# Kernel optimization log

Hardware: AMD Instinct MI355X
Metric: run time of the kernel (lower is better)

Reference implementation:

```python
import jax, jax.numpy as jnp
import numpy as np

KH = KW = 3
STRIDE = 2
PAD = 1


def _extract_patches(x, kh, kw, stride, pad):
    # x: [B, C, H, W] -> patches [B, C, Ho, Wo, kh*kw]
    B, C, H, W = x.shape
    xp = jnp.pad(x, ((0, 0), (0, 0), (pad, pad), (pad, pad)))
    Ho = (H + 2 * pad - kh) // stride + 1
    Wo = (W + 2 * pad - kw) // stride + 1
    cols = [
        xp[:, :, i : i + stride * Ho : stride, j : j + stride * Wo : stride]
        for i in range(kh)
        for j in range(kw)
    ]
    return jnp.stack(cols, axis=-1)  # [B, C, Ho, Wo, kh*kw]


def setup_inputs() -> dict:
    key = jax.random.key(0)
    k1, k2 = jax.random.split(key)
    x = jax.random.normal(k1, (32, 64, 112, 112), dtype=jnp.float32)
    s = jax.random.normal(k2, (64, KH, KW), dtype=jnp.float32) * 0.1
    return {"x": x, "s": s}


def reference(x, s):
    # RRSVM rank-weighted pooling: for each sliding window, sort values
    # descending and take a weighted sum with per-channel rank weights s.
    patches = _extract_patches(x, KH, KW, STRIDE, PAD)  # [B,C,Ho,Wo,K]
    order = jnp.argsort(-patches, axis=-1)              # descending ranks
    sorted_vals = jnp.take_along_axis(patches, order, axis=-1)
    s_flat = s.reshape(s.shape[0], KH * KW)             # [C, K]
    out = jnp.einsum("bchwk,ck->bchw", sorted_vals, s_flat)
    return out, order.astype(jnp.int64)
```

## Files before the change

kernel.cpp:

```cpp
#include <hip/hip_runtime.h>


typedef float nfloat4 __attribute__((ext_vector_type(4)));

constexpr int B  = 32;
constexpr int C  = 64;
constexpr int H  = 112;
constexpr int W  = 112;
constexpr int HO = 56;
constexpr int WO = 56;
constexpr int KK = 9;
constexpr int NPIX = HO * WO;
constexpr int BLK  = 256;
constexpr int LROW = 128;
constexpr int RPT  = 4;
constexpr int IR   = 2 * RPT + 1;

__global__ __launch_bounds__(BLK) void rrsvm_kernel(
    const float* __restrict__ x, const float* __restrict__ s,
    float* __restrict__ out, float* __restrict__ order)
{
    __shared__ float lx[IR * LROW];
    __shared__ float lorder[RPT * WO * KK];

    const int plane = blockIdx.y;
    const int ho0   = blockIdx.x;
    const int tid   = threadIdx.x;
    const int w     = tid >> 6;
    const int lane  = tid & 63;
    const int c     = plane & (C - 1);

    const float* xp = x + (size_t)plane * (H * W);

    if (tid < IR * (W / 4)) {
        const int r  = tid / (W / 4);
        const int cc = tid - r * (W / 4);
        const int grow = 8 * ho0 - 1 + r;
        nfloat4 val = (nfloat4)0.0f;
        if ((unsigned)grow < (unsigned)H)
            val = *(const nfloat4*)(xp + grow * W + 4 * cc);
        float* dst = &lx[r * LROW + 1 + 4 * cc];
        dst[0] = val.x; dst[1] = val.y; dst[2] = val.z; dst[3] = val.w;
    }
    if (tid < IR) lx[tid * LROW] = 0.0f;
    __syncthreads();

    const bool live = (lane < WO);
    const int  lc   = live ? lane : 0;
    const int  ho   = ho0 * RPT + w;

    float v[KK];
    float fid[KK];
#pragma unroll
    for (int dy = 0; dy < 3; ++dy)
#pragma unroll
        for (int dx = 0; dx < 3; ++dx) {
            const int k = dy * 3 + dx;
            v[k]   = lx[(2 * w + dy) * LROW + 2 * lc + dx];
            fid[k] = (float)k;
        }

    auto CE = [&](int a, int b) {
        const float va = v[a],   vb = v[b];
        const float fa = fid[a], fb = fid[b];
        const bool sw = (va < vb) || ((va == vb) && (fa > fb));
        v[a]   = sw ? vb : va;  v[b]   = sw ? va : vb;
        fid[a] = sw ? fb : fa;  fid[b] = sw ? fa : fb;
    };
    CE(0,1); CE(2,3); CE(4,5); CE(6,7);
    CE(0,2); CE(1,3); CE(4,6); CE(5,7);
    CE(1,2); CE(5,6);
    CE(0,4); CE(1,5); CE(2,6); CE(3,7);
    CE(2,4); CE(3,5);
    CE(1,2); CE(3,4); CE(5,6);
    CE(7,8); CE(6,7); CE(5,6); CE(4,5); CE(3,4); CE(2,3); CE(1,2); CE(0,1);

    const float* sc = s + c * KK;
    float acc = 0.0f;
#pragma unroll
    for (int k = 0; k < KK; ++k) acc = fmaf(v[k], sc[k], acc);

    if (live) {
        __builtin_nontemporal_store(acc, out + (size_t)plane * NPIX + ho * WO + lane);
        const int widx = w * WO + lane;
#pragma unroll
        for (int k = 0; k < KK; ++k)
            lorder[widx * KK + k] = fid[k];
    }
    __syncthreads();

    nfloat4* __restrict__ ob =
        (nfloat4*)(order + ((size_t)plane * NPIX + (size_t)ho0 * RPT * WO) * KK);
    const nfloat4* __restrict__ lb = (const nfloat4*)lorder;
#pragma unroll
    for (int i = tid; i < RPT * WO * KK / 4; i += BLK)
        __builtin_nontemporal_store(lb[i], ob + i);
}

extern "C" void kernel_launch(void* const* d_in, const int* in_sizes, int n_in,
                              void* d_out, int out_size, void* d_ws, size_t ws_size,
                              hipStream_t stream) {
    const float* x = (const float*)d_in[0];
    const float* s = (const float*)d_in[1];
    float* out   = (float*)d_out;
    float* order = out + (size_t)B * C * NPIX;

    dim3 grid(HO / RPT, B * C);
    rrsvm_kernel<<<grid, dim3(BLK), 0, stream>>>(x, s, out, order);
}
```

Baseline: 313.3 us.

## Make each block loop over all row tiles of a plane with double-buffered staging

The grid changes from one block per (row-tile, plane) to one persistent block per plane, which iterates over all 14 row tiles. The next tile's input rows are prefetched into registers during compute and written to the alternate LDS buffer, so load latency can overlap with sorting and stores. Per-channel weights are loaded once per block, and the halo rows between tiles are re-read. The cost is a grid of only 2048 blocks, which means less parallelism and longer-running blocks, plus two barriers per iteration.

```diff
diff --git a/kernel.cpp b/kernel.cpp
--- a/kernel.cpp
+++ b/kernel.cpp
@@ -15,16 +15,16 @@
 constexpr int LROW = 128;
 constexpr int RPT  = 4;
 constexpr int IR   = 2 * RPT + 1;
+constexpr int NT   = HO / RPT;
 
-__global__ __launch_bounds__(BLK) void rrsvm_kernel(
+__global__ __launch_bounds__(BLK, 8) void rrsvm_kernel(
     const float* __restrict__ x, const float* __restrict__ s,
     float* __restrict__ out, float* __restrict__ order)
 {
-    __shared__ float lx[IR * LROW];
+    __shared__ float lx[2][IR * LROW];
     __shared__ float lorder[RPT * WO * KK];
 
-    const int plane = blockIdx.y;
-    const int ho0   = blockIdx.x;
+    const int plane = blockIdx.x;
     const int tid   = threadIdx.x;
     const int w     = tid >> 6;
     const int lane  = tid & 63;
@@ -32,69 +32,94 @@
 
     const float* xp = x + (size_t)plane * (H * W);
 
-    if (tid < IR * (W / 4)) {
-        const int r  = tid / (W / 4);
-        const int cc = tid - r * (W / 4);
-        const int grow = 8 * ho0 - 1 + r;
+    const bool stager = (tid < IR * (W / 4));
+    const int  sr  = tid / (W / 4);
+    const int  scc = tid - sr * (W / 4);
+
+    float wts[KK];
+#pragma unroll
+    for (int k = 0; k < KK; ++k) wts[k] = s[c * KK + k];
+
+    if (tid < 2 * IR) {
+        const int bi = tid / IR, r = tid - bi * IR;
+        lx[bi][r * LROW] = 0.0f;
+    }
+
+    if (stager) {
+        const int grow = sr - 1;
         nfloat4 val = (nfloat4)0.0f;
         if ((unsigned)grow < (unsigned)H)
-            val = *(const nfloat4*)(xp + grow * W + 4 * cc);
-        float* dst = &lx[r * LROW + 1 + 4 * cc];
+            val = *(const nfloat4*)(xp + grow * W + 4 * scc);
+        float* dst = &lx[0][sr * LROW + 1 + 4 * scc];
         dst[0] = val.x; dst[1] = val.y; dst[2] = val.z; dst[3] = val.w;
     }
-    if (tid < IR) lx[tid * LROW] = 0.0f;
     __syncthreads();
 
     const bool live = (lane < WO);
     const int  lc   = live ? lane : 0;
-    const int  ho   = ho0 * RPT + w;
 
-    float v[KK];
-    float fid[KK];
-#pragma unroll
-    for (int dy = 0; dy < 3; ++dy)
-#pragma unroll
-        for (int dx = 0; dx < 3; ++dx) {
-            const int k = dy * 3 + dx;
-            v[k]   = lx[(2 * w + dy) * LROW + 2 * lc + dx];
-            fid[k] = (float)k;
+    for (int t = 0; t < NT; ++t) {
+        nfloat4 nval = (nfloat4)0.0f;
+        if (t + 1 < NT && stager) {
+            const int grow = 8 * (t + 1) - 1 + sr;
+            nval = *(const nfloat4*)(xp + grow * W + 4 * scc);
         }
 
-    auto CE = [&](int a, int b) {
-        const float va = v[a],   vb = v[b];
-        const float fa = fid[a], fb = fid[b];
-        const bool sw = (va < vb) || ((va == vb) && (fa > fb));
-        v[a]   = sw ? vb : va;  v[b]   = sw ? va : vb;
-        fid[a] = sw ? fb : fa;  fid[b] = sw ? fa : fb;
-    };
-    CE(0,1); CE(2,3); CE(4,5); CE(6,7);
-    CE(0,2); CE(1,3); CE(4,6); CE(5,7);
-    CE(1,2); CE(5,6);
-    CE(0,4); CE(1,5); CE(2,6); CE(3,7);
-    CE(2,4); CE(3,5);
-    CE(1,2); CE(3,4); CE(5,6);
-    CE(7,8); CE(6,7); CE(5,6); CE(4,5); CE(3,4); CE(2,3); CE(1,2); CE(0,1);
+        const float* lxt = lx[t & 1];
+        float v[KK];
+        float fid[KK];
+#pragma unroll
+        for (int dy = 0; dy < 3; ++dy)
+#pragma unroll
+            for (int dx = 0; dx < 3; ++dx) {
+                const int k = dy * 3 + dx;
+                v[k]   = lxt[(2 * w + dy) * LROW + 2 * lc + dx];
+                fid[k] = (float)k;
+            }
 
-    const float* sc = s + c * KK;
-    float acc = 0.0f;
+        auto CE = [&](int a, int b) {
+            const float va = v[a],   vb = v[b];
+            const float fa = fid[a], fb = fid[b];
+            const bool sw = (va < vb) || ((va == vb) && (fa > fb));
+            v[a]   = sw ? vb : va;  v[b]   = sw ? va : vb;
+            fid[a] = sw ? fb : fa;  fid[b] = sw ? fa : fb;
+        };
+        CE(0,1); CE(2,3); CE(4,5); CE(6,7);
+        CE(0,2); CE(1,3); CE(4,6); CE(5,7);
+        CE(1,2); CE(5,6);
+        CE(0,4); CE(1,5); CE(2,6); CE(3,7);
+        CE(2,4); CE(3,5);
+        CE(1,2); CE(3,4); CE(5,6);
+        CE(7,8); CE(6,7); CE(5,6); CE(4,5); CE(3,4); CE(2,3); CE(1,2); CE(0,1);
+
+        float acc = 0.0f;
 #pragma unroll
-    for (int k = 0; k < KK; ++k) acc = fmaf(v[k], sc[k], acc);
+        for (int k = 0; k < KK; ++k) acc = fmaf(v[k], wts[k], acc);
 
-    if (live) {
-        __builtin_nontemporal_store(acc, out + (size_t)plane * NPIX + ho * WO + lane);
-        const int widx = w * WO + lane;
+        const int ho = t * RPT + w;
+        if (live) {
+            __builtin_nontemporal_store(
+                acc, out + (size_t)plane * NPIX + ho * WO + lane);
+            const int widx = w * WO + lane;
 #pragma unroll
-        for (int k = 0; k < KK; ++k)
-            lorder[widx * KK + k] = fid[k];
+            for (int k = 0; k < KK; ++k)
+                lorder[widx * KK + k] = fid[k];
+        }
+        __syncthreads();
+
+        nfloat4* __restrict__ ob =
+            (nfloat4*)(order + ((size_t)plane * NPIX + (size_t)t * RPT * WO) * KK);
+        const nfloat4* __restrict__ lb = (const nfloat4*)lorder;
+#pragma unroll
+        for (int i = tid; i < RPT * WO * KK / 4; i += BLK)
+            __builtin_nontemporal_store(lb[i], ob + i);
+
+        if (t + 1 < NT && stager) {
+            float* dst = &lx[(t + 1) & 1][sr * LROW + 1 + 4 * scc];
+            dst[0] = nval.x; dst[1] = nval.y; dst[2] = nval.z; dst[3] = nval.w;
+        }
+        __syncthreads();
     }
-    __syncthreads();
-
-    nfloat4* __restrict__ ob =
-        (nfloat4*)(order + ((size_t)plane * NPIX + (size_t)ho0 * RPT * WO) * KK);
-    const nfloat4* __restrict__ lb = (const nfloat4*)lorder;
-#pragma unroll
-    for (int i = tid; i < RPT * WO * KK / 4; i += BLK)
-        __builtin_nontemporal_store(lb[i], ob + i);
 }
 
 extern "C" void kernel_launch(void* const* d_in, const int* in_sizes, int n_in,
@@ -105,6 +130,6 @@
     float* out   = (float*)d_out;
     float* order = out + (size_t)B * C * NPIX;
 
-    dim3 grid(HO / RPT, B * C);
+    dim3 grid(B * C);
     rrsvm_kernel<<<grid, dim3(BLK), 0, stream>>>(x, s, out, order);
 }
```

After: 339.8 us. +8.5%, slower.
